# Kernel optimization log

Measured on AMD Instinct MI355X. Metric: run time of the kernel, lower is better.

## Reference

```python
import jax, jax.numpy as jnp
import numpy as np

DIM = 512
NUM_HEADS = 8
HEAD_DIM = DIM // NUM_HEADS
EPS = 1e-12  # F.normalize default eps


def _l2norm(x):
    # F.normalize: x / max(||x||_2, eps) along last dim
    n = jnp.sqrt(jnp.sum(x * x, axis=-1, keepdims=True))
    return x / jnp.maximum(n, EPS)


def setup_inputs() -> dict:
    key = jax.random.key(0)
    ks = jax.random.split(key, 7)
    B, N, K = 8, 4096, 256
    scale = 1.0 / np.sqrt(DIM)
    return {
        "X_flat": jax.random.normal(ks[0], (B, N, DIM), jnp.float32),
        "S_tokens": jax.random.normal(ks[1], (B, K, DIM), jnp.float32),
        "Wq": jax.random.normal(ks[2], (DIM, DIM), jnp.float32) * scale,
        "Wk": jax.random.normal(ks[3], (DIM, DIM), jnp.float32) * scale,
        "Wv": jax.random.normal(ks[4], (DIM, DIM), jnp.float32) * scale,
        "Wo": jax.random.normal(ks[5], (DIM, DIM), jnp.float32) * scale,
        "temperature": jnp.ones((NUM_HEADS, 1, 1), jnp.float32),
    }


def reference(X_flat, S_tokens, Wq, Wk, Wv, Wo, temperature):
    B, N, C = X_flat.shape
    K = S_tokens.shape[1]
    H, D = NUM_HEADS, HEAD_DIM
    # torch Linear: y = x @ W.T
    q = (X_flat @ Wq.T).reshape(B, N, H, D).transpose(0, 2, 1, 3)   # (B,H,N,D)
    k = (S_tokens @ Wk.T).reshape(B, K, H, D).transpose(0, 2, 1, 3)  # (B,H,K,D)
    v = (S_tokens @ Wv.T).reshape(B, K, H, D).transpose(0, 2, 1, 3)  # (B,H,K,D)
    q = _l2norm(q)
    k = _l2norm(k)
    attn = jnp.einsum('bhnd,bhkd->bhnk', q, k) * temperature  # temperature (H,1,1) broadcasts
    attn = jax.nn.softmax(attn, axis=-1)
    out = jnp.einsum('bhnk,bhkd->bhnd', attn, v)
    out = out.transpose(0, 2, 1, 3).reshape(B, N, C)
    out = out @ Wo.T
    return X_flat + out
```

## Files before the change

### kernel.cpp

```cpp
#include <hip/hip_runtime.h>
#include <hip/hip_bf16.h>


typedef __bf16 bf16;
typedef __attribute__((ext_vector_type(8))) __bf16 bf16x8;
typedef __attribute__((ext_vector_type(4))) float f32x4;

__device__ __forceinline__ void gload_lds16(const void* g, void* l) {
  __builtin_amdgcn_global_load_lds(
      (__attribute__((address_space(1))) void*)g,
      (__attribute__((address_space(3))) void*)l, 16, 0, 0);
}

__device__ __forceinline__ unsigned pack2(float a, float b) {
  unsigned short x = __builtin_bit_cast(unsigned short, (bf16)a);
  unsigned short y = __builtin_bit_cast(unsigned short, (bf16)b);
  return (unsigned)x | ((unsigned)y << 16);
}

__global__ __launch_bounds__(256) void cvt_all(
    const float* __restrict__ X, const float* __restrict__ S,
    const float* __restrict__ Wq, const float* __restrict__ Wk,
    const float* __restrict__ Wv, const float* __restrict__ Wo,
    bf16* __restrict__ Xb, bf16* __restrict__ Sb, bf16* __restrict__ Wqb,
    bf16* __restrict__ Wkb, bf16* __restrict__ Wvb, bf16* __restrict__ Wob) {
  int i = blockIdx.x * 256 + threadIdx.x;
  const float* src;
  bf16* dst;
  int r;
  if (i < 2097152) {
    src = X; dst = Xb; r = i;
  } else if (i < 2228224) {
    src = S; dst = Sb; r = i - 2097152;
  } else {
    int j = i - 2228224;
    int w = j >> 15;
    r = j & 32767;
    src = (w == 0) ? Wq : (w == 1) ? Wk : (w == 2) ? Wv : Wo;
    dst = (w == 0) ? Wqb : (w == 1) ? Wkb : (w == 2) ? Wvb : Wob;
  }
  float4 a = *(const float4*)(src + (size_t)r * 8);
  float4 b = *(const float4*)(src + (size_t)r * 8 + 4);
  uint4 v;
  v.x = pack2(a.x, a.y);
  v.y = pack2(a.z, a.w);
  v.z = pack2(b.x, b.y);
  v.w = pack2(b.z, b.w);
  *(uint4*)(dst + (size_t)r * 8) = v;
}

__global__ __launch_bounds__(256) void proj_all(
    const bf16* __restrict__ Xb, const bf16* __restrict__ Sb,
    const bf16* __restrict__ Wqb, const bf16* __restrict__ Wkb,
    const bf16* __restrict__ Wvb, bf16* __restrict__ Q,
    bf16* __restrict__ Kn, bf16* __restrict__ Vt) {
  __shared__ __align__(16) char smem[49152];

  const int lg = (blockIdx.x & 7) * 144 + (blockIdx.x >> 3);

  const bf16* A;
  const bf16* W;
  int m0, kind;
  if (lg < 1024) {
    kind = 0; A = Xb; W = Wqb; m0 = (lg >> 2) * 128;
  } else if (lg < 1088) {
    kind = 1; A = Sb; W = Wkb; m0 = ((lg - 1024) >> 2) * 128;
  } else {
    kind = 2; A = Sb; W = Wvb; m0 = ((lg - 1088) >> 2) * 128;
  }
  const int n0 = (lg & 3) * 128;

  const int tid = threadIdx.x;
  const int wid = tid >> 6, lane = tid & 63;
  const int wr = wid >> 1, wc = wid & 1;
  const int g = lane >> 4, c16 = lane & 15;
  const int r0 = tid >> 2, cc0 = tid & 3;
  const int r1 = (256 + tid) >> 2, cc1 = tid & 3;
  const int dst0 = (tid & ~63) * 16, dst1 = (256 + (tid & ~63)) * 16;

  f32x4 acc[4][4] = {};

#define PSTAGE(kb, buf)                                                     \
  {                                                                         \
    char* as = smem + (buf) * 8192;                                         \
    char* bs = smem + 24576 + (buf) * 8192;                                 \
    gload_lds16(A + (size_t)(m0 + r0) * 512 + (kb) + cc0 * 8, as + dst0);   \
    gload_lds16(A + (size_t)(m0 + r1) * 512 + (kb) + cc1 * 8, as + dst1);   \
    gload_lds16(W + (size_t)(n0 + r0) * 512 + (kb) + cc0 * 8, bs + dst0);   \
    gload_lds16(W + (size_t)(n0 + r1) * 512 + (kb) + cc1 * 8, bs + dst1);   \
  }

#define PCOMPUTE(buf)                                                       \
  {                                                                         \
    const bf16* as = (const bf16*)(smem + (buf) * 8192);                    \
    const bf16* bs = (const bf16*)(smem + 24576 + (buf) * 8192);            \
    bf16x8 af[4], bfr[4];                                                   \
    _Pragma("unroll") for (int mi = 0; mi < 4; ++mi) af[mi] =               \
        *(const bf16x8*)(as + (wr * 64 + mi * 16 + c16) * 32 + g * 8);      \
    _Pragma("unroll") for (int ni = 0; ni < 4; ++ni) bfr[ni] =              \
        *(const bf16x8*)(bs + (wc * 64 + ni * 16 + c16) * 32 + g * 8);      \
    _Pragma("unroll") for (int mi = 0; mi < 4; ++mi)                        \
        _Pragma("unroll") for (int ni = 0; ni < 4; ++ni) acc[mi][ni] =      \
            __builtin_amdgcn_mfma_f32_16x16x32_bf16(af[mi], bfr[ni],        \
                                                    acc[mi][ni], 0, 0, 0);  \
  }

  PSTAGE(0, 0);
  PSTAGE(32, 1);
  int bufc = 0;
  for (int t = 0; t < 14; ++t) {
    int bufn = bufc + 2;
    if (bufn >= 3) bufn -= 3;
    PSTAGE((t + 2) * 32, bufn);
    asm volatile("s_waitcnt vmcnt(8)" ::: "memory");
    __builtin_amdgcn_s_barrier();
    PCOMPUTE(bufc);
    __builtin_amdgcn_s_barrier();
    if (++bufc == 3) bufc = 0;
  }
  asm volatile("s_waitcnt vmcnt(4)" ::: "memory");
  __builtin_amdgcn_s_barrier();
  PCOMPUTE(bufc);
  __builtin_amdgcn_s_barrier();
  if (++bufc == 3) bufc = 0;
  asm volatile("s_waitcnt vmcnt(0)" ::: "memory");
  __builtin_amdgcn_s_barrier();
  PCOMPUTE(bufc);

  __syncthreads();

  if (kind != 2) {
    bf16* C = (kind == 0) ? Q : Kn;
    char* eps = smem + wid * 8192;
#pragma unroll
    for (int mi = 0; mi < 4; ++mi) {
      float ss[4];
#pragma unroll
      for (int j = 0; j < 4; ++j) {
        float s = 0.f;
#pragma unroll
        for (int ni = 0; ni < 4; ++ni) {
          float v = acc[mi][ni][j];
          s += v * v;
        }
        ss[j] = s;
      }
#pragma unroll
      for (int msk = 1; msk < 16; msk <<= 1)
#pragma unroll
        for (int j = 0; j < 4; ++j) ss[j] += __shfl_xor(ss[j], msk, 64);
      float inv[4];
#pragma unroll
      for (int j = 0; j < 4; ++j) inv[j] = rsqrtf(fmaxf(ss[j], 1e-24f));
#pragma unroll
      for (int ni = 0; ni < 4; ++ni)
#pragma unroll
        for (int j = 0; j < 4; ++j) {
          int row = mi * 16 + g * 4 + j, col = ni * 16 + c16;
          int off = (row * 128 + col * 2) ^ ((row & 7) << 4);
          *(bf16*)(eps + off) = (bf16)(acc[mi][ni][j] * inv[j]);
        }
    }
    asm volatile("s_waitcnt lgkmcnt(0)" ::: "memory");
#pragma unroll
    for (int it = 0; it < 8; ++it) {
      int c = it * 64 + lane;
      int row = c >> 3, ch = c & 7;
      int off = (row * 128 + ch * 16) ^ ((row & 7) << 4);
      bf16x8 v = *(const bf16x8*)(eps + off);
      *(bf16x8*)(C + (size_t)(m0 + wr * 64 + row) * 512 + n0 + wc * 64 +
                 ch * 8) = v;
    }
  } else {
#pragma unroll
    for (int mi = 0; mi < 4; ++mi) {
      int m = m0 + wr * 64 + mi * 16 + g * 4;
      int b = m >> 8, tt = m & 255;
#pragma unroll
      for (int ni = 0; ni < 4; ++ni) {
        int col = n0 + wc * 64 + ni * 16 + c16;
        int h = col >> 6, d = col & 63;
        uint2 v;
        v.x = pack2(acc[mi][ni][0], acc[mi][ni][1]);
        v.y = pack2(acc[mi][ni][2], acc[mi][ni][3]);
        *(uint2*)(Vt + ((size_t)((b * 8 + h) * 64 + d) * 256 + tt)) = v;
      }
    }
  }
#undef PSTAGE
#undef PCOMPUTE
}

__global__ __launch_bounds__(256) void out_gemm(
    const bf16* __restrict__ O, const bf16* __restrict__ Wob,
    const float* __restrict__ Xres, float* __restrict__ out) {
  __shared__ __align__(16) char smem[49152];

  const int lg = (blockIdx.x & 7) * 128 + (blockIdx.x >> 3);
  const int m0 = (lg >> 2) * 128, n0 = (lg & 3) * 128;

  const int tid = threadIdx.x;
  const int wid = tid >> 6, lane = tid & 63;
  const int wr = wid >> 1, wc = wid & 1;
  const int g = lane >> 4, c16 = lane & 15;
  const int r0 = tid >> 2, cc0 = tid & 3;
  const int r1 = (256 + tid) >> 2, cc1 = tid & 3;
  const int dst0 = (tid & ~63) * 16, dst1 = (256 + (tid & ~63)) * 16;

  f32x4 acc[4][4] = {};

#define OSTAGE(kb, buf)                                                      \
  {                                                                          \
    char* as = smem + (buf) * 8192;                                          \
    char* bs = smem + 24576 + (buf) * 8192;                                  \
    gload_lds16(O + (size_t)(m0 + r0) * 512 + (kb) + cc0 * 8, as + dst0);    \
    gload_lds16(O + (size_t)(m0 + r1) * 512 + (kb) + cc1 * 8, as + dst1);    \
    gload_lds16(Wob + (size_t)(n0 + r0) * 512 + (kb) + cc0 * 8, bs + dst0);  \
    gload_lds16(Wob + (size_t)(n0 + r1) * 512 + (kb) + cc1 * 8, bs + dst1);  \
  }

#define OCOMPUTE(buf)                                                       \
  {                                                                         \
    const bf16* as = (const bf16*)(smem + (buf) * 8192);                    \
    const bf16* bs = (const bf16*)(smem + 24576 + (buf) * 8192);            \
    bf16x8 af[4], bfr[4];                                                   \
    _Pragma("unroll") for (int mi = 0; mi < 4; ++mi) af[mi] =               \
        *(const bf16x8*)(as + (wr * 64 + mi * 16 + c16) * 32 + g * 8);      \
    _Pragma("unroll") for (int ni = 0; ni < 4; ++ni) bfr[ni] =              \
        *(const bf16x8*)(bs + (wc * 64 + ni * 16 + c16) * 32 + g * 8);      \
    _Pragma("unroll") for (int mi = 0; mi < 4; ++mi)                        \
        _Pragma("unroll") for (int ni = 0; ni < 4; ++ni) acc[mi][ni] =      \
            __builtin_amdgcn_mfma_f32_16x16x32_bf16(af[mi], bfr[ni],        \
                                                    acc[mi][ni], 0, 0, 0);  \
  }

  OSTAGE(0, 0);
  OSTAGE(32, 1);
  int bufc = 0;
  for (int t = 0; t < 14; ++t) {
    int bufn = bufc + 2;
    if (bufn >= 3) bufn -= 3;
    OSTAGE((t + 2) * 32, bufn);
    asm volatile("s_waitcnt vmcnt(8)" ::: "memory");
    __builtin_amdgcn_s_barrier();
    OCOMPUTE(bufc);
    __builtin_amdgcn_s_barrier();
    if (++bufc == 3) bufc = 0;
  }
  asm volatile("s_waitcnt vmcnt(4)" ::: "memory");
  __builtin_amdgcn_s_barrier();
  OCOMPUTE(bufc);
  __builtin_amdgcn_s_barrier();
  if (++bufc == 3) bufc = 0;
  asm volatile("s_waitcnt vmcnt(0)" ::: "memory");
  __builtin_amdgcn_s_barrier();
  OCOMPUTE(bufc);

  __syncthreads();

  char* eps = smem + wid * 8192;
#pragma unroll
  for (int p = 0; p < 2; ++p) {
#pragma unroll
    for (int mm = 0; mm < 2; ++mm)
#pragma unroll
      for (int ni = 0; ni < 4; ++ni)
#pragma unroll
        for (int j = 0; j < 4; ++j) {
          int row = mm * 16 + g * 4 + j, col = ni * 16 + c16;
          int off = (row * 256 + col * 4) ^ ((row & 7) << 4);
          *(float*)(eps + off) = acc[p * 2 + mm][ni][j];
        }
    asm volatile("s_waitcnt lgkmcnt(0)" ::: "memory");
#pragma unroll
    for (int it = 0; it < 8; ++it) {
      int c = it * 64 + lane;
      int row = c >> 4, ch = c & 15;
      int off = (row * 256 + ch * 16) ^ ((row & 7) << 4);
      float4 v = *(const float4*)(eps + off);
      size_t gr = (size_t)(m0 + wr * 64 + p * 32 + row) * 512 + n0 +
                  wc * 64 + ch * 4;
      float4 x = *(const float4*)(Xres + gr);
      v.x += x.x;
      v.y += x.y;
      v.z += x.z;
      v.w += x.w;
      *(float4*)(out + gr) = v;
    }
    asm volatile("s_waitcnt lgkmcnt(0)" ::: "memory");
  }
#undef OSTAGE
#undef OCOMPUTE
}

__global__ __launch_bounds__(512) void attn_fused(
    const bf16* __restrict__ Qn, const bf16* __restrict__ Kn,
    const bf16* __restrict__ Vt, const float* __restrict__ temp,
    bf16* __restrict__ O) {
  __shared__ __align__(16) char smem[147456];

  const int tid = threadIdx.x;
  const int w = tid >> 6, lane = tid & 63;
  const int g = lane >> 4, c16 = lane & 15;
  const int bx = blockIdx.x;
  const int nt = bx & 31, h = (bx >> 5) & 7, b = bx >> 8;
  const int n0 = nt * 128;

  {
    const bf16* Ksrc = Kn + ((size_t)b * 256) * 512 + h * 64;
#pragma unroll
    for (int it = 0; it < 4; ++it) {
      int c = it * 512 + tid;
      int t = c >> 3, dc = c & 7;
      int4 v = *(const int4*)(Ksrc + (size_t)t * 512 + dc * 8);
      int off = (t * 128 + dc * 16) ^ ((t & 7) << 4);
      *(int4*)(smem + off) = v;
    }
    const bf16* Vsrc = Vt + (size_t)((b * 8 + h) * 64) * 256;
#pragma unroll
    for (int it = 0; it < 4; ++it) {
      int c = it * 512 + tid;
      int d = c >> 5, tc = c & 31;
      int4 v = *(const int4*)(Vsrc + (size_t)d * 256 + tc * 8);
      int off = (d * 512 + tc * 16) ^ ((d & 7) << 4);
      *(int4*)(smem + 32768 + off) = v;
    }
    const bf16* Qsrc = Qn + ((size_t)b * 4096 + n0) * 512 + h * 64;
#pragma unroll
    for (int it = 0; it < 2; ++it) {
      int c = it * 512 + tid;
      int q = c >> 3, dc = c & 7;
      int4 v = *(const int4*)(Qsrc + (size_t)q * 512 + dc * 8);
      int off = (q * 128 + dc * 16) ^ ((q & 7) << 4);
      *(int4*)(smem + 65536 + off) = v;
    }
  }
  __syncthreads();

  const int q = w * 16 + c16;

  f32x4 sacc[16] = {};
  bf16x8 qf[2];
#pragma unroll
  for (int s = 0; s < 2; ++s) {
    int off = (q * 128 + s * 64 + g * 16) ^ ((q & 7) << 4);
    qf[s] = *(const bf16x8*)(smem + 65536 + off);
  }
#pragma unroll
  for (int mi = 0; mi < 16; ++mi) {
#pragma unroll
    for (int s = 0; s < 2; ++s) {
      int t = mi * 16 + c16;
      int off = (t * 128 + s * 64 + g * 16) ^ ((t & 7) << 4);
      bf16x8 kf = *(const bf16x8*)(smem + off);
      sacc[mi] = __builtin_amdgcn_mfma_f32_16x16x32_bf16(kf, qf[s], sacc[mi],
                                                         0, 0, 0);
    }
  }

  float tv = temp[h];
  float mx = -1e30f;
#pragma unroll
  for (int mi = 0; mi < 16; ++mi)
#pragma unroll
    for (int j = 0; j < 4; ++j) {
      sacc[mi][j] *= tv;
      mx = fmaxf(mx, sacc[mi][j]);
    }
  mx = fmaxf(mx, __shfl_xor(mx, 16, 64));
  mx = fmaxf(mx, __shfl_xor(mx, 32, 64));
  float sum = 0.f;
#pragma unroll
  for (int mi = 0; mi < 16; ++mi)
#pragma unroll
    for (int j = 0; j < 4; ++j) {
      float p = __expf(sacc[mi][j] - mx);
      sacc[mi][j] = p;
      sum += p;
    }
  sum += __shfl_xor(sum, 16, 64);
  sum += __shfl_xor(sum, 32, 64);
  float inv = 1.0f / sum;

#pragma unroll
  for (int mi = 0; mi < 16; ++mi) {
    uint2 v;
    v.x = pack2(sacc[mi][0] * inv, sacc[mi][1] * inv);
    v.y = pack2(sacc[mi][2] * inv, sacc[mi][3] * inv);
    int off = (q * 512 + mi * 32 + g * 8) ^ ((q & 7) << 4);
    *(uint2*)(smem + 81920 + off) = v;
  }
  __syncthreads();

  f32x4 oacc[4] = {};
#pragma unroll
  for (int ks = 0; ks < 8; ++ks) {
    int offa = (q * 512 + ks * 64 + g * 16) ^ ((q & 7) << 4);
    bf16x8 pa = *(const bf16x8*)(smem + 81920 + offa);
#pragma unroll
    for (int ni = 0; ni < 4; ++ni) {
      int d = ni * 16 + c16;
      int offb = (d * 512 + ks * 64 + g * 16) ^ ((d & 7) << 4);
      bf16x8 vb = *(const bf16x8*)(smem + 32768 + offb);
      oacc[ni] = __builtin_amdgcn_mfma_f32_16x16x32_bf16(pa, vb, oacc[ni],
                                                         0, 0, 0);
    }
  }

  {
    char* ox = smem + 65536 + w * 2048;
#pragma unroll
    for (int ni = 0; ni < 4; ++ni)
#pragma unroll
      for (int j = 0; j < 4; ++j) {
        int row = g * 4 + j, col = ni * 16 + c16;
        int off = (row * 128 + col * 2) ^ ((row & 7) << 4);
        *(bf16*)(ox + off) = (bf16)oacc[ni][j];
      }
    asm volatile("s_waitcnt lgkmcnt(0)" ::: "memory");
#pragma unroll
    for (int it = 0; it < 2; ++it) {
      int c = it * 64 + lane;
      int row = c >> 3, ch = c & 7;
      int off = (row * 128 + ch * 16) ^ ((row & 7) << 4);
      bf16x8 v = *(const bf16x8*)(ox + off);
      *(bf16x8*)(O + ((size_t)b * 4096 + n0 + w * 16 + row) * 512 + h * 64 +
                 ch * 8) = v;
    }
  }
}

extern "C" void kernel_launch(void* const* d_in, const int* in_sizes, int n_in,
                              void* d_out, int out_size, void* d_ws,
                              size_t ws_size, hipStream_t stream) {
  const float* X = (const float*)d_in[0];
  const float* S = (const float*)d_in[1];
  const float* Wq = (const float*)d_in[2];
  const float* Wk = (const float*)d_in[3];
  const float* Wv = (const float*)d_in[4];
  const float* Wo = (const float*)d_in[5];
  const float* temp = (const float*)d_in[6];
  float* out = (float*)d_out;

  char* ws = (char*)d_ws;
  bf16* Qws = (bf16*)ws;
  bf16* Kws = (bf16*)(ws + 33554432);
  bf16* Vtws = (bf16*)(ws + 35651584);
  bf16* Wqb = (bf16*)(ws + 37748736);
  bf16* Wkb = (bf16*)(ws + 38273024);
  bf16* Wvb = (bf16*)(ws + 38797312);
  bf16* Wob = (bf16*)(ws + 39321600);

  bf16* Xb = (bf16*)d_out;
  bf16* Sb = (bf16*)((char*)d_out + 33554432);

  cvt_all<<<dim3(9216), dim3(256), 0, stream>>>(X, S, Wq, Wk, Wv, Wo, Xb, Sb,
                                                Wqb, Wkb, Wvb, Wob);
  proj_all<<<dim3(1152), dim3(256), 0, stream>>>(Xb, Sb, Wqb, Wkb, Wvb, Qws,
                                                 Kws, Vtws);
  attn_fused<<<dim3(2048), dim3(512), 0, stream>>>(Qws, Kws, Vtws, temp, Qws);
  out_gemm<<<dim3(1024), dim3(256), 0, stream>>>(Qws, Wob, X, out);
}
```

Baseline: 134.9 us.

## Halve attention block size and reuse K smem for probabilities to raise occupancy

```diff
diff --git a/kernel.cpp b/kernel.cpp
--- a/kernel.cpp
+++ b/kernel.cpp
@@ -293,24 +293,24 @@
 #undef OCOMPUTE
 }
 
-__global__ __launch_bounds__(512) void attn_fused(
+__global__ __launch_bounds__(256) void attn_fused(
     const bf16* __restrict__ Qn, const bf16* __restrict__ Kn,
     const bf16* __restrict__ Vt, const float* __restrict__ temp,
     bf16* __restrict__ O) {
-  __shared__ __align__(16) char smem[147456];
+  __shared__ __align__(16) char smem[73728];
 
   const int tid = threadIdx.x;
   const int w = tid >> 6, lane = tid & 63;
   const int g = lane >> 4, c16 = lane & 15;
-  const int bx = blockIdx.x;
-  const int nt = bx & 31, h = (bx >> 5) & 7, b = bx >> 8;
-  const int n0 = nt * 128;
+  const int lg = (blockIdx.x & 7) * 512 + (blockIdx.x >> 3);
+  const int nt = lg & 63, h = (lg >> 6) & 7, b = lg >> 9;
+  const int n0 = nt * 64;
 
   {
     const bf16* Ksrc = Kn + ((size_t)b * 256) * 512 + h * 64;
 #pragma unroll
-    for (int it = 0; it < 4; ++it) {
-      int c = it * 512 + tid;
+    for (int it = 0; it < 8; ++it) {
+      int c = it * 256 + tid;
       int t = c >> 3, dc = c & 7;
       int4 v = *(const int4*)(Ksrc + (size_t)t * 512 + dc * 8);
       int off = (t * 128 + dc * 16) ^ ((t & 7) << 4);
@@ -318,8 +318,8 @@
     }
     const bf16* Vsrc = Vt + (size_t)((b * 8 + h) * 64) * 256;
 #pragma unroll
-    for (int it = 0; it < 4; ++it) {
-      int c = it * 512 + tid;
+    for (int it = 0; it < 8; ++it) {
+      int c = it * 256 + tid;
       int d = c >> 5, tc = c & 31;
       int4 v = *(const int4*)(Vsrc + (size_t)d * 256 + tc * 8);
       int off = (d * 512 + tc * 16) ^ ((d & 7) << 4);
@@ -328,11 +328,11 @@
     const bf16* Qsrc = Qn + ((size_t)b * 4096 + n0) * 512 + h * 64;
 #pragma unroll
     for (int it = 0; it < 2; ++it) {
-      int c = it * 512 + tid;
+      int c = it * 256 + tid;
       int q = c >> 3, dc = c & 7;
       int4 v = *(const int4*)(Qsrc + (size_t)q * 512 + dc * 8);
-      int off = (q * 128 + dc * 16) ^ ((q & 7) << 4);
-      *(int4*)(smem + 65536 + off) = v;
+      int off = 65536 + ((q * 128 + dc * 16) ^ ((q & 7) << 4));
+      *(int4*)(smem + off) = v;
     }
   }
   __syncthreads();
@@ -343,8 +343,8 @@
   bf16x8 qf[2];
 #pragma unroll
   for (int s = 0; s < 2; ++s) {
-    int off = (q * 128 + s * 64 + g * 16) ^ ((q & 7) << 4);
-    qf[s] = *(const bf16x8*)(smem + 65536 + off);
+    int off = 65536 + ((q * 128 + s * 64 + g * 16) ^ ((q & 7) << 4));
+    qf[s] = *(const bf16x8*)(smem + off);
   }
 #pragma unroll
   for (int mi = 0; mi < 16; ++mi) {
@@ -359,28 +359,32 @@
   }
 
   float tv = temp[h];
-  float mx = -1e30f;
+  float mx4[4] = {-1e30f, -1e30f, -1e30f, -1e30f};
 #pragma unroll
   for (int mi = 0; mi < 16; ++mi)
 #pragma unroll
     for (int j = 0; j < 4; ++j) {
       sacc[mi][j] *= tv;
-      mx = fmaxf(mx, sacc[mi][j]);
-    }
+      mx4[j] = fmaxf(mx4[j], sacc[mi][j]);
+    }
+  float mx = fmaxf(fmaxf(mx4[0], mx4[1]), fmaxf(mx4[2], mx4[3]));
   mx = fmaxf(mx, __shfl_xor(mx, 16, 64));
   mx = fmaxf(mx, __shfl_xor(mx, 32, 64));
-  float sum = 0.f;
+  float sm4[4] = {0.f, 0.f, 0.f, 0.f};
 #pragma unroll
   for (int mi = 0; mi < 16; ++mi)
 #pragma unroll
     for (int j = 0; j < 4; ++j) {
       float p = __expf(sacc[mi][j] - mx);
       sacc[mi][j] = p;
-      sum += p;
-    }
+      sm4[j] += p;
+    }
+  float sum = (sm4[0] + sm4[1]) + (sm4[2] + sm4[3]);
   sum += __shfl_xor(sum, 16, 64);
   sum += __shfl_xor(sum, 32, 64);
   float inv = 1.0f / sum;
+
+  __syncthreads();
 
 #pragma unroll
   for (int mi = 0; mi < 16; ++mi) {
@@ -388,7 +392,7 @@
     v.x = pack2(sacc[mi][0] * inv, sacc[mi][1] * inv);
     v.y = pack2(sacc[mi][2] * inv, sacc[mi][3] * inv);
     int off = (q * 512 + mi * 32 + g * 8) ^ ((q & 7) << 4);
-    *(uint2*)(smem + 81920 + off) = v;
+    *(uint2*)(smem + off) = v;
   }
   __syncthreads();
 
@@ -396,12 +400,12 @@
 #pragma unroll
   for (int ks = 0; ks < 8; ++ks) {
     int offa = (q * 512 + ks * 64 + g * 16) ^ ((q & 7) << 4);
-    bf16x8 pa = *(const bf16x8*)(smem + 81920 + offa);
+    bf16x8 pa = *(const bf16x8*)(smem + offa);
 #pragma unroll
     for (int ni = 0; ni < 4; ++ni) {
       int d = ni * 16 + c16;
-      int offb = (d * 512 + ks * 64 + g * 16) ^ ((d & 7) << 4);
-      bf16x8 vb = *(const bf16x8*)(smem + 32768 + offb);
+      int offb = 32768 + ((d * 512 + ks * 64 + g * 16) ^ ((d & 7) << 4));
+      bf16x8 vb = *(const bf16x8*)(smem + offb);
       oacc[ni] = __builtin_amdgcn_mfma_f32_16x16x32_bf16(pa, vb, oacc[ni],
                                                          0, 0, 0);
     }
@@ -458,6 +462,6 @@
                                                 Wqb, Wkb, Wvb, Wob);
   proj_all<<<dim3(1152), dim3(256), 0, stream>>>(Xb, Sb, Wqb, Wkb, Wvb, Qws,
                                                  Kws, Vtws);
-  attn_fused<<<dim3(2048), dim3(512), 0, stream>>>(Qws, Kws, Vtws, temp, Qws);
+  attn_fused<<<dim3(4096), dim3(256), 0, stream>>>(Qws, Kws, Vtws, temp, Qws);
   out_gemm<<<dim3(1024), dim3(256), 0, stream>>>(Qws, Wob, X, out);
 }
```

Result: faster. 129.6 us (-3.9%).
